# Optimization experiments

Measured on AMD Instinct MI355X. Metric: run time of the kernel, lower is better.

Reference implementation:

```python
import jax, jax.numpy as jnp
import numpy as np

N = 50000      # nodes
E = 800000     # edges (avg degree 16)
D = 128        # d_model
H = 8          # num_heads
DK = D // H    # d_k = 16


def setup_inputs() -> dict:
    key = jax.random.key(0)
    ks = jax.random.split(key, 9)
    scale = np.float32(1.0 / np.sqrt(D))
    return {
        "q": jax.random.normal(ks[0], (N, D), jnp.float32),
        "k": jax.random.normal(ks[1], (N, D), jnp.float32),
        "v": jax.random.normal(ks[2], (N, D), jnp.float32),
        "e": jax.random.normal(ks[3], (E, D), jnp.float32),
        "src": jax.random.randint(ks[4], (E,), 0, N),
        "dst": jax.random.randint(ks[5], (E,), 0, N),
        # nn.Linear(D, D, bias=False) weights, stored as [in, out]
        "Wq": jax.random.normal(ks[6], (D, D), jnp.float32) * scale,
        "Wk": jax.random.normal(ks[7], (D, D), jnp.float32) * scale,
        "Wv": jax.random.normal(ks[8], (D, D), jnp.float32) * scale,
    }


def reference(q, k, v, e, src, dst, Wq, Wk, Wv):
    inv_sqrt_dk = np.float32(1.0 / np.sqrt(DK))
    # node-level V projection, then per-edge gather of src V  -> [E, H, DK]
    Vn = (v @ Wv).reshape(N, H, DK)
    Ve = Vn[src]
    # per-edge Q from dst node, K from (src k + edge feature e)
    Qe = (q[dst] @ Wq).reshape(E, H, DK)
    Ke = ((k[src] + e) @ Wk).reshape(E, H, DK)
    # per-edge HxH score matrix: Q @ K^T / sqrt(d_k), leaky-relu
    s = jnp.einsum("ehd,egd->ehg", Qe, Ke) * inv_sqrt_dk   # [E, H, H]
    s = jax.nn.leaky_relu(s)
    # softmax over last head axis (within each edge, as in reduce_func dim=-1)
    A = jax.nn.softmax(s, axis=-1)
    # per-edge message, heads regrouped -> [E, D]
    He = jnp.einsum("ehg,egd->ehd", A, Ve).reshape(E, D)
    # plain sum over incoming edges per destination node -> [N, D]
    return jax.ops.segment_sum(He, dst, num_segments=N)
```

## Files before the change

kernel.cpp:

```cpp
#include <hip/hip_runtime.h>
#include <hip/hip_bf16.h>
#include <math.h>

#define NN 50000
#define EE 800000
#define DD 128
#define HH 8
#define DKK 16

typedef __attribute__((ext_vector_type(8))) short short8;
typedef __attribute__((ext_vector_type(4))) float f32x4;
typedef __attribute__((ext_vector_type(4))) unsigned short ushort4v;
typedef __attribute__((ext_vector_type(8))) unsigned short ushort8v;

static __device__ __forceinline__ unsigned short f2bf(float x) {
  __hip_bfloat16 h = __float2bfloat16(x);
  return *reinterpret_cast<unsigned short*>(&h);
}
static __device__ __forceinline__ float bf2f(unsigned short u) {
  return __uint_as_float(((unsigned int)u) << 16);
}

__global__ __launch_bounds__(256) void hist_kernel(const int* __restrict__ dst,
                                                   int* __restrict__ cnt) {
  int i4 = blockIdx.x * 256 + threadIdx.x;
  if (i4 < EE / 4) {
    int4 d = *(const int4*)&dst[i4 * 4];
    atomicAdd(&cnt[d.x], 1);
    atomicAdd(&cnt[d.y], 1);
    atomicAdd(&cnt[d.z], 1);
    atomicAdd(&cnt[d.w], 1);
  }
}

#define SCAN_NB ((NN + 1023) / 1024)

__global__ __launch_bounds__(256) void scan1_kernel(const int* __restrict__ cnt,
                                                    int* __restrict__ bsum) {
  __shared__ int red[256];
  const int b = blockIdx.x, t = threadIdx.x;
  const int base = b * 1024 + t * 4;
  int s = 0;
  if (base + 3 < NN) {
    int4 v = *(const int4*)&cnt[base];
    s = v.x + v.y + v.z + v.w;
  } else {
    for (int j = 0; j < 4; ++j) if (base + j < NN) s += cnt[base + j];
  }
  red[t] = s;
  __syncthreads();
  for (int off = 1; off < 256; off <<= 1) {
    int v = (t >= off) ? red[t - off] : 0;
    __syncthreads();
    red[t] += v;
    __syncthreads();
  }
  if (t == 255) bsum[b] = red[255];
}

__global__ __launch_bounds__(256) void scan3_kernel(const int* __restrict__ cnt,
                                                    const int* __restrict__ bsum,
                                                    int* __restrict__ rowptr) {
  __shared__ int red[256];
  __shared__ int bs[SCAN_NB];
  const int b = blockIdx.x, t = threadIdx.x;
  if (t < SCAN_NB) bs[t] = bsum[t];
  const int base = b * 1024 + t * 4;
  int v0 = 0, v1 = 0, v2 = 0, v3 = 0;
  if (base + 3 < NN) {
    int4 v = *(const int4*)&cnt[base];
    v0 = v.x; v1 = v.y; v2 = v.z; v3 = v.w;
  } else {
    if (base + 0 < NN) v0 = cnt[base + 0];
    if (base + 1 < NN) v1 = cnt[base + 1];
    if (base + 2 < NN) v2 = cnt[base + 2];
    if (base + 3 < NN) v3 = cnt[base + 3];
  }
  red[t] = v0 + v1 + v2 + v3;
  __syncthreads();
  for (int off = 1; off < 256; off <<= 1) {
    int v = (t >= off) ? red[t - off] : 0;
    __syncthreads();
    red[t] += v;
    __syncthreads();
  }
  int bpre = 0;
  for (int j = 0; j < b; ++j) bpre += bs[j];
  int r = bpre + ((t == 0) ? 0 : red[t - 1]);
  if (base + 0 < NN) { rowptr[base + 0] = r; r += v0; }
  if (base + 1 < NN) { rowptr[base + 1] = r; r += v1; }
  if (base + 2 < NN) { rowptr[base + 2] = r; r += v2; }
  if (base + 3 < NN) { rowptr[base + 3] = r; }
}

__global__ __launch_bounds__(256) void fill_kernel(const int* __restrict__ dst,
                                                   const int* __restrict__ rowptr,
                                                   int* __restrict__ cur,
                                                   int* __restrict__ perm) {
  int i4 = blockIdx.x * 256 + threadIdx.x;
  if (i4 < EE / 4) {
    int4 dv = *(const int4*)&dst[i4 * 4];
    int d0 = dv.x, d1 = dv.y, d2 = dv.z, d3 = dv.w;
    int s0 = atomicAdd(&cur[d0], 1); perm[rowptr[d0] + s0] = i4 * 4 + 0;
    int s1 = atomicAdd(&cur[d1], 1); perm[rowptr[d1] + s1] = i4 * 4 + 1;
    int s2 = atomicAdd(&cur[d2], 1); perm[rowptr[d2] + s2] = i4 * 4 + 2;
    int s3 = atomicAdd(&cur[d3], 1); perm[rowptr[d3] + s3] = i4 * 4 + 3;
  }
}

__global__ void prep_w_kernel(const float* __restrict__ Wq,
                              const float* __restrict__ Wk,
                              const float* __restrict__ Wv,
                              unsigned short* __restrict__ WqT,
                              unsigned short* __restrict__ WkT,
                              unsigned short* __restrict__ WvT) {
  int c = blockIdx.x & 127;
  int m = blockIdx.x >> 7;
  int j = threadIdx.x;
  const float* W = (m == 0) ? Wq : (m == 1) ? Wk : Wv;
  unsigned short* o = (m == 0) ? WqT : (m == 1) ? WkT : WvT;
  o[j * DD + c] = f2bf(W[c * DD + j]);
}

__global__ __launch_bounds__(512) void node_proj_kernel(
    const float* __restrict__ q, const float* __restrict__ v,
    const float* __restrict__ k,
    const unsigned short* __restrict__ WqT, const unsigned short* __restrict__ WvT,
    unsigned short* __restrict__ Qh, unsigned short* __restrict__ Vh,
    unsigned short* __restrict__ kh)
{
  __shared__ __align__(16) unsigned short xl[64 * 136];
  const int tid = threadIdx.x;
  const int n0 = blockIdx.x * 64;

  #pragma unroll
  for (int p = 0; p < 2; ++p) {
    int f = p * 512 + tid;
    int i = f >> 4, c8 = f & 15;
    int n = n0 + i;
    if (n < NN) {
      float4 a = *(const float4*)&k[(size_t)n * DD + c8 * 8];
      float4 b = *(const float4*)&k[(size_t)n * DD + c8 * 8 + 4];
      ushort8v o = { f2bf(a.x), f2bf(a.y), f2bf(a.z), f2bf(a.w),
                     f2bf(b.x), f2bf(b.y), f2bf(b.z), f2bf(b.w) };
      *(ushort8v*)&kh[(size_t)n * DD + c8 * 8] = o;
    }
  }

  for (int m = 0; m < 2; ++m) {
    const float* x = m ? v : q;
    const unsigned short* WT = m ? WvT : WqT;
    unsigned short* o = m ? Vh : Qh;

    __syncthreads();
    #pragma unroll
    for (int p = 0; p < 4; ++p) {
      int f = p * 512 + tid;
      int i = f >> 5, c4 = f & 31;
      int n = n0 + i;
      float4 t = (n < NN) ? *(const float4*)&x[(size_t)n * DD + c4 * 4]
                          : float4{0.f, 0.f, 0.f, 0.f};
      ushort4v u = { f2bf(t.x), f2bf(t.y), f2bf(t.z), f2bf(t.w) };
      *(ushort4v*)&xl[i * 136 + c4 * 4] = u;
    }
    __syncthreads();

    const int lane = tid & 63, wid = tid >> 6;
    const int rg = wid & 3, cg = wid >> 2;
    const int lr = lane & 15, lg = lane >> 4;

    f32x4 acc0 = {0.f,0.f,0.f,0.f}, acc1 = {0.f,0.f,0.f,0.f};
    f32x4 acc2 = {0.f,0.f,0.f,0.f}, acc3 = {0.f,0.f,0.f,0.f};

    const unsigned short* Ab = &xl[(rg * 16 + lr) * 136];
    const unsigned short* B0 = &WT[(size_t)(cg * 64 +  0 + lr) * DD];
    const unsigned short* B1 = &WT[(size_t)(cg * 64 + 16 + lr) * DD];
    const unsigned short* B2 = &WT[(size_t)(cg * 64 + 32 + lr) * DD];
    const unsigned short* B3 = &WT[(size_t)(cg * 64 + 48 + lr) * DD];

    #pragma unroll
    for (int kk = 0; kk < 4; ++kk) {
      const int kof = kk * 32 + lg * 8;
      short8 a = *(const short8*)(Ab + kof);
      acc0 = __builtin_amdgcn_mfma_f32_16x16x32_bf16(a, *(const short8*)(B0 + kof), acc0, 0, 0, 0);
      acc1 = __builtin_amdgcn_mfma_f32_16x16x32_bf16(a, *(const short8*)(B1 + kof), acc1, 0, 0, 0);
      acc2 = __builtin_amdgcn_mfma_f32_16x16x32_bf16(a, *(const short8*)(B2 + kof), acc2, 0, 0, 0);
      acc3 = __builtin_amdgcn_mfma_f32_16x16x32_bf16(a, *(const short8*)(B3 + kof), acc3, 0, 0, 0);
    }

    const int r0 = rg * 16 + lg * 4;
    const int cb = cg * 64 + lr;
    #pragma unroll
    for (int r = 0; r < 4; ++r) {
      int n = n0 + r0 + r;
      if (n < NN) {
        unsigned short* orow = &o[(size_t)n * DD + cb];
        orow[ 0] = f2bf(acc0[r]);
        orow[16] = f2bf(acc1[r]);
        orow[32] = f2bf(acc2[r]);
        orow[48] = f2bf(acc3[r]);
      }
    }
  }
}

__global__ __launch_bounds__(512, 4) void edge_attn_kernel(
    const unsigned short* __restrict__ kh, const float* __restrict__ e,
    const int* __restrict__ src, const int* __restrict__ dst,
    const int* __restrict__ perm,
    const unsigned short* __restrict__ WkT,
    const unsigned short* __restrict__ Qh, const unsigned short* __restrict__ Vh,
    float* __restrict__ out)
{
  __shared__ __align__(16) unsigned short buf[128 * 136];
  __shared__ __align__(16) unsigned short vbuf[128 * 136];
  __shared__ __align__(16) unsigned short pbuf[8 * 16 * 24];
  __shared__ int s_perm[128], s_src[128], s_dst[128];

  const int tid = threadIdx.x;
  const size_t e0 = (size_t)blockIdx.x * 128;
  const int lane = tid & 63, wid = tid >> 6;
  const int lr = lane & 15, lg = lane >> 4;

  if (tid < 128) {
    int pe = perm[e0 + tid];
    s_perm[tid] = pe;
    s_src[tid] = src[pe];
    s_dst[tid] = dst[pe];
  }
  __syncthreads();

  ushort8v vv[4], kv[4];
  float4 ea[4], eb[4];
  #pragma unroll
  for (int p = 0; p < 4; ++p) {
    int f = p * 512 + tid;
    int i2 = f >> 4, c8 = f & 15;
    vv[p] = *(const ushort8v*)&Vh[(size_t)s_src[i2] * DD + c8 * 8];
    kv[p] = *(const ushort8v*)&kh[(size_t)s_src[i2] * DD + c8 * 8];
    const float* ep = &e[(size_t)s_perm[i2] * DD + c8 * 8];
    ea[p] = *(const float4*)ep;
    eb[p] = *(const float4*)(ep + 4);
  }

  const short8 zero8 = {0, 0, 0, 0, 0, 0, 0, 0};
  const int ebase = wid * 16;
  short8 qf[8];
  #pragma unroll
  for (int j = 0; j < 8; ++j) {
    if (lg < 2) {
      int ie = ebase + 2 * j + (lr >> 3);
      qf[j] = *(const short8*)&Qh[(size_t)s_dst[ie] * DD + (lr & 7) * DKK + lg * 8];
    } else qf[j] = zero8;
  }

  #pragma unroll
  for (int p = 0; p < 4; ++p) {
    int f = p * 512 + tid;
    int i2 = f >> 4, c8 = f & 15;
    *(ushort8v*)&vbuf[i2 * 136 + c8 * 8] = vv[p];
    ushort8v o;
    o[0] = f2bf(bf2f(kv[p][0]) + ea[p].x);
    o[1] = f2bf(bf2f(kv[p][1]) + ea[p].y);
    o[2] = f2bf(bf2f(kv[p][2]) + ea[p].z);
    o[3] = f2bf(bf2f(kv[p][3]) + ea[p].w);
    o[4] = f2bf(bf2f(kv[p][4]) + eb[p].x);
    o[5] = f2bf(bf2f(kv[p][5]) + eb[p].y);
    o[6] = f2bf(bf2f(kv[p][6]) + eb[p].z);
    o[7] = f2bf(bf2f(kv[p][7]) + eb[p].w);
    *(ushort8v*)&buf[i2 * 136 + c8 * 8] = o;
  }
  __syncthreads();

  {
    const int rgA = wid & 3, rgB = (wid & 3) + 4, cg = wid >> 2;

    f32x4 aA0 = {0.f,0.f,0.f,0.f}, aA1 = {0.f,0.f,0.f,0.f};
    f32x4 aA2 = {0.f,0.f,0.f,0.f}, aA3 = {0.f,0.f,0.f,0.f};
    f32x4 aB0 = {0.f,0.f,0.f,0.f}, aB1 = {0.f,0.f,0.f,0.f};
    f32x4 aB2 = {0.f,0.f,0.f,0.f}, aB3 = {0.f,0.f,0.f,0.f};

    const unsigned short* AbA = &buf[(rgA * 16 + lr) * 136];
    const unsigned short* AbB = &buf[(rgB * 16 + lr) * 136];
    const unsigned short* B0 = &WkT[(size_t)(cg * 64 +  0 + lr) * DD];
    const unsigned short* B1 = &WkT[(size_t)(cg * 64 + 16 + lr) * DD];
    const unsigned short* B2 = &WkT[(size_t)(cg * 64 + 32 + lr) * DD];
    const unsigned short* B3 = &WkT[(size_t)(cg * 64 + 48 + lr) * DD];

    #pragma unroll
    for (int kk = 0; kk < 4; ++kk) {
      const int kof = kk * 32 + lg * 8;
      short8 b0 = *(const short8*)(B0 + kof);
      short8 b1 = *(const short8*)(B1 + kof);
      short8 b2 = *(const short8*)(B2 + kof);
      short8 b3 = *(const short8*)(B3 + kof);
      short8 fA = *(const short8*)(AbA + kof);
      short8 fB = *(const short8*)(AbB + kof);
      aA0 = __builtin_amdgcn_mfma_f32_16x16x32_bf16(fA, b0, aA0, 0, 0, 0);
      aA1 = __builtin_amdgcn_mfma_f32_16x16x32_bf16(fA, b1, aA1, 0, 0, 0);
      aA2 = __builtin_amdgcn_mfma_f32_16x16x32_bf16(fA, b2, aA2, 0, 0, 0);
      aA3 = __builtin_amdgcn_mfma_f32_16x16x32_bf16(fA, b3, aA3, 0, 0, 0);
      aB0 = __builtin_amdgcn_mfma_f32_16x16x32_bf16(fB, b0, aB0, 0, 0, 0);
      aB1 = __builtin_amdgcn_mfma_f32_16x16x32_bf16(fB, b1, aB1, 0, 0, 0);
      aB2 = __builtin_amdgcn_mfma_f32_16x16x32_bf16(fB, b2, aB2, 0, 0, 0);
      aB3 = __builtin_amdgcn_mfma_f32_16x16x32_bf16(fB, b3, aB3, 0, 0, 0);
    }

    __syncthreads();

    const int rA = rgA * 16 + lg * 4;
    const int rB = rgB * 16 + lg * 4;
    const int cb = cg * 64 + lr;
    #pragma unroll
    for (int r = 0; r < 4; ++r) {
      buf[(rA + r) * 136 + cb +  0] = f2bf(aA0[r]);
      buf[(rA + r) * 136 + cb + 16] = f2bf(aA1[r]);
      buf[(rA + r) * 136 + cb + 32] = f2bf(aA2[r]);
      buf[(rA + r) * 136 + cb + 48] = f2bf(aA3[r]);
      buf[(rB + r) * 136 + cb +  0] = f2bf(aB0[r]);
      buf[(rB + r) * 136 + cb + 16] = f2bf(aB1[r]);
      buf[(rB + r) * 136 + cb + 32] = f2bf(aB2[r]);
      buf[(rB + r) * 136 + cb + 48] = f2bf(aB3[r]);
    }
  }
  __syncthreads();

  {
    const bool valid = ((lr < 8) == (lg < 2));
    unsigned short* pb = &pbuf[wid * 16 * 24];

    #pragma unroll
    for (int j = 0; j < 8; ++j) {
      const int iea = ebase + 2 * j, ieb = iea + 1;

      short8 af = zero8;
      if (lg < 2) {
        int ie = (lr < 8) ? iea : ieb;
        af = *(const short8*)&buf[ie * 136 + (lr & 7) * DKK + lg * 8];
      }
      f32x4 c = {0.f, 0.f, 0.f, 0.f};
      c = __builtin_amdgcn_mfma_f32_16x16x32_bf16(af, qf[j], c, 0, 0, 0);

      float s0, s1, s2, s3;
      {
        float x0 = c[0] * 0.25f, x1 = c[1] * 0.25f;
        float x2 = c[2] * 0.25f, x3 = c[3] * 0.25f;
        x0 = (x0 >= 0.f) ? x0 : 0.01f * x0;
        x1 = (x1 >= 0.f) ? x1 : 0.01f * x1;
        x2 = (x2 >= 0.f) ? x2 : 0.01f * x2;
        x3 = (x3 >= 0.f) ? x3 : 0.01f * x3;
        s0 = valid ? x0 : -1e30f;
        s1 = valid ? x1 : -1e30f;
        s2 = valid ? x2 : -1e30f;
        s3 = valid ? x3 : -1e30f;
      }
      float m = fmaxf(fmaxf(s0, s1), fmaxf(s2, s3));
      m = fmaxf(m, __shfl_xor(m, 16));
      m = fmaxf(m, __shfl_xor(m, 32));
      float p0 = __expf(s0 - m), p1 = __expf(s1 - m);
      float p2 = __expf(s2 - m), p3 = __expf(s3 - m);
      float su = p0 + p1 + p2 + p3;
      su += __shfl_xor(su, 16);
      su += __shfl_xor(su, 32);
      float rs = 1.0f / su;

      ushort4v pk = { f2bf(p0 * rs), f2bf(p1 * rs), f2bf(p2 * rs), f2bf(p3 * rs) };
      *(ushort4v*)&pb[lr * 24 + lg * 4] = pk;

      short8 pa = zero8;
      if (lg < 2) pa = *(const short8*)&pb[lr * 24 + lg * 8];
      short8 vf = zero8;
      if (lg < 2) {
        const unsigned short* vr = &vbuf[(lg ? ieb : iea) * 136 + lr];
        vf[0] = (short)vr[0 * 16];
        vf[1] = (short)vr[1 * 16];
        vf[2] = (short)vr[2 * 16];
        vf[3] = (short)vr[3 * 16];
        vf[4] = (short)vr[4 * 16];
        vf[5] = (short)vr[5 * 16];
        vf[6] = (short)vr[6 * 16];
        vf[7] = (short)vr[7 * 16];
      }
      f32x4 hc = {0.f, 0.f, 0.f, 0.f};
      hc = __builtin_amdgcn_mfma_f32_16x16x32_bf16(pa, vf, hc, 0, 0, 0);

      #pragma unroll
      for (int r = 0; r < 4; ++r) {
        int rr = lg * 4 + r;
        int ie = (rr < 8) ? iea : ieb;
        buf[ie * 136 + (rr & 7) * DKK + lr] = f2bf(hc[r]);
      }
    }
  }

  {
    const int d2 = lane;
    const int base = ebase;
    float s0 = 0.0f, s1 = 0.0f;
    int curd = s_dst[base];
    #pragma unroll 8
    for (int j = 0; j < 16; ++j) {
      int i2 = base + j;
      int dn2 = s_dst[i2];
      if (dn2 != curd) {
        atomicAdd(&out[(size_t)curd * DD + d2 * 2],     s0);
        atomicAdd(&out[(size_t)curd * DD + d2 * 2 + 1], s1);
        s0 = 0.0f; s1 = 0.0f;
        curd = dn2;
      }
      unsigned int w = *(const unsigned int*)&buf[i2 * 136 + d2 * 2];
      s0 += bf2f((unsigned short)(w & 0xffff));
      s1 += bf2f((unsigned short)(w >> 16));
    }
    atomicAdd(&out[(size_t)curd * DD + d2 * 2],     s0);
    atomicAdd(&out[(size_t)curd * DD + d2 * 2 + 1], s1);
  }
}

extern "C" void kernel_launch(void* const* d_in, const int* in_sizes, int n_in,
                              void* d_out, int out_size, void* d_ws, size_t ws_size,
                              hipStream_t stream) {
  const float* q  = (const float*)d_in[0];
  const float* k  = (const float*)d_in[1];
  const float* v  = (const float*)d_in[2];
  const float* e  = (const float*)d_in[3];
  const int*   src = (const int*)d_in[4];
  const int*   dst = (const int*)d_in[5];
  const float* Wq = (const float*)d_in[6];
  const float* Wk = (const float*)d_in[7];
  const float* Wv = (const float*)d_in[8];

  float* out = (float*)d_out;
  char* wsb = (char*)d_ws;
  unsigned short* Qh  = (unsigned short*)wsb;
  unsigned short* Vh  = Qh + (size_t)NN * DD;
  unsigned short* kh  = Vh + (size_t)NN * DD;
  unsigned short* WqT = kh + (size_t)NN * DD;
  unsigned short* WkT = WqT + DD * DD;
  unsigned short* WvT = WkT + DD * DD;
  int* cnt    = (int*)(WvT + DD * DD);
  int* cur    = cnt + NN;
  int* rowptr = cur + NN;
  int* bsum   = rowptr + NN + 1;
  int* perm   = bsum + 64;

  hipMemsetAsync(d_out, 0, (size_t)NN * DD * sizeof(float), stream);
  hipMemsetAsync(cnt, 0, 2 * NN * sizeof(int), stream);

  hist_kernel <<<(EE / 4 + 255) / 256, 256, 0, stream>>>(dst, cnt);
  scan1_kernel<<<SCAN_NB, 256, 0, stream>>>(cnt, bsum);
  scan3_kernel<<<SCAN_NB, 256, 0, stream>>>(cnt, bsum, rowptr);
  fill_kernel <<<(EE / 4 + 255) / 256, 256, 0, stream>>>(dst, rowptr, cur, perm);

  prep_w_kernel<<<3 * DD, DD, 0, stream>>>(Wq, Wk, Wv, WqT, WkT, WvT);
  node_proj_kernel<<<(NN + 63) / 64, 512, 0, stream>>>(q, v, k, WqT, WvT,
                                                       Qh, Vh, kh);
  edge_attn_kernel<<<EE / 128, 512, 0, stream>>>(kh, e, src, dst, perm,
                                                 WkT, Qh, Vh, out);
}
```

Measured before the change: 384.5 us.

## Halve edge tile to 64 per block and fuse gather with K+e store

The edge attention kernel now processes 64 edges per 512-thread block instead of 128. Shared memory per block halves and the launch-bounds occupancy hint is dropped. The gather loop writes V and K+e into shared memory right away instead of holding all loads in registers first, which lowers register pressure. In exchange each block reuses the WkT tile over fewer edges, segment runs for the atomic reductions are shorter, and there are twice as many blocks.

After: 416.2 us. +8.2%, slower.

```diff
diff --git a/kernel.cpp b/kernel.cpp
--- a/kernel.cpp
+++ b/kernel.cpp
@@ -204,7 +204,7 @@
   }
 }
 
-__global__ __launch_bounds__(512, 4) void edge_attn_kernel(
+__global__ __launch_bounds__(512) void edge_attn_kernel(
     const unsigned short* __restrict__ kh, const float* __restrict__ e,
     const int* __restrict__ src, const int* __restrict__ dst,
     const int* __restrict__ perm,
@@ -212,17 +212,17 @@
     const unsigned short* __restrict__ Qh, const unsigned short* __restrict__ Vh,
     float* __restrict__ out)
 {
-  __shared__ __align__(16) unsigned short buf[128 * 136];
-  __shared__ __align__(16) unsigned short vbuf[128 * 136];
+  __shared__ __align__(16) unsigned short buf[64 * 136];
+  __shared__ __align__(16) unsigned short vbuf[64 * 136];
   __shared__ __align__(16) unsigned short pbuf[8 * 16 * 24];
-  __shared__ int s_perm[128], s_src[128], s_dst[128];
+  __shared__ int s_perm[64], s_src[64], s_dst[64];
 
   const int tid = threadIdx.x;
-  const size_t e0 = (size_t)blockIdx.x * 128;
+  const size_t e0 = (size_t)blockIdx.x * 64;
   const int lane = tid & 63, wid = tid >> 6;
   const int lr = lane & 15, lg = lane >> 4;
 
-  if (tid < 128) {
+  if (tid < 64) {
     int pe = perm[e0 + tid];
     s_perm[tid] = pe;
     s_src[tid] = src[pe];
@@ -230,58 +230,47 @@
   }
   __syncthreads();
 
-  ushort8v vv[4], kv[4];
-  float4 ea[4], eb[4];
   #pragma unroll
-  for (int p = 0; p < 4; ++p) {
+  for (int p = 0; p < 2; ++p) {
     int f = p * 512 + tid;
     int i2 = f >> 4, c8 = f & 15;
-    vv[p] = *(const ushort8v*)&Vh[(size_t)s_src[i2] * DD + c8 * 8];
-    kv[p] = *(const ushort8v*)&kh[(size_t)s_src[i2] * DD + c8 * 8];
+    ushort8v vv = *(const ushort8v*)&Vh[(size_t)s_src[i2] * DD + c8 * 8];
+    ushort8v kv = *(const ushort8v*)&kh[(size_t)s_src[i2] * DD + c8 * 8];
     const float* ep = &e[(size_t)s_perm[i2] * DD + c8 * 8];
-    ea[p] = *(const float4*)ep;
-    eb[p] = *(const float4*)(ep + 4);
+    float4 ea = *(const float4*)ep;
+    float4 eb = *(const float4*)(ep + 4);
+    *(ushort8v*)&vbuf[i2 * 136 + c8 * 8] = vv;
+    ushort8v o;
+    o[0] = f2bf(bf2f(kv[0]) + ea.x);
+    o[1] = f2bf(bf2f(kv[1]) + ea.y);
+    o[2] = f2bf(bf2f(kv[2]) + ea.z);
+    o[3] = f2bf(bf2f(kv[3]) + ea.w);
+    o[4] = f2bf(bf2f(kv[4]) + eb.x);
+    o[5] = f2bf(bf2f(kv[5]) + eb.y);
+    o[6] = f2bf(bf2f(kv[6]) + eb.z);
+    o[7] = f2bf(bf2f(kv[7]) + eb.w);
+    *(ushort8v*)&buf[i2 * 136 + c8 * 8] = o;
   }
 
   const short8 zero8 = {0, 0, 0, 0, 0, 0, 0, 0};
-  const int ebase = wid * 16;
-  short8 qf[8];
+  const int ebase = wid * 8;
+  short8 qf[4];
   #pragma unroll
-  for (int j = 0; j < 8; ++j) {
+  for (int j = 0; j < 4; ++j) {
     if (lg < 2) {
       int ie = ebase + 2 * j + (lr >> 3);
       qf[j] = *(const short8*)&Qh[(size_t)s_dst[ie] * DD + (lr & 7) * DKK + lg * 8];
     } else qf[j] = zero8;
   }
-
-  #pragma unroll
-  for (int p = 0; p < 4; ++p) {
-    int f = p * 512 + tid;
-    int i2 = f >> 4, c8 = f & 15;
-    *(ushort8v*)&vbuf[i2 * 136 + c8 * 8] = vv[p];
-    ushort8v o;
-    o[0] = f2bf(bf2f(kv[p][0]) + ea[p].x);
-    o[1] = f2bf(bf2f(kv[p][1]) + ea[p].y);
-    o[2] = f2bf(bf2f(kv[p][2]) + ea[p].z);
-    o[3] = f2bf(bf2f(kv[p][3]) + ea[p].w);
-    o[4] = f2bf(bf2f(kv[p][4]) + eb[p].x);
-    o[5] = f2bf(bf2f(kv[p][5]) + eb[p].y);
-    o[6] = f2bf(bf2f(kv[p][6]) + eb[p].z);
-    o[7] = f2bf(bf2f(kv[p][7]) + eb[p].w);
-    *(ushort8v*)&buf[i2 * 136 + c8 * 8] = o;
-  }
   __syncthreads();
 
   {
-    const int rgA = wid & 3, rgB = (wid & 3) + 4, cg = wid >> 2;
-
-    f32x4 aA0 = {0.f,0.f,0.f,0.f}, aA1 = {0.f,0.f,0.f,0.f};
-    f32x4 aA2 = {0.f,0.f,0.f,0.f}, aA3 = {0.f,0.f,0.f,0.f};
-    f32x4 aB0 = {0.f,0.f,0.f,0.f}, aB1 = {0.f,0.f,0.f,0.f};
-    f32x4 aB2 = {0.f,0.f,0.f,0.f}, aB3 = {0.f,0.f,0.f,0.f};
-
-    const unsigned short* AbA = &buf[(rgA * 16 + lr) * 136];
-    const unsigned short* AbB = &buf[(rgB * 16 + lr) * 136];
+    const int rg = wid & 3, cg = wid >> 2;
+
+    f32x4 a0 = {0.f,0.f,0.f,0.f}, a1 = {0.f,0.f,0.f,0.f};
+    f32x4 a2 = {0.f,0.f,0.f,0.f}, a3 = {0.f,0.f,0.f,0.f};
+
+    const unsigned short* Ab = &buf[(rg * 16 + lr) * 136];
     const unsigned short* B0 = &WkT[(size_t)(cg * 64 +  0 + lr) * DD];
     const unsigned short* B1 = &WkT[(size_t)(cg * 64 + 16 + lr) * DD];
     const unsigned short* B2 = &WkT[(size_t)(cg * 64 + 32 + lr) * DD];
@@ -290,37 +279,23 @@
     #pragma unroll
     for (int kk = 0; kk < 4; ++kk) {
       const int kof = kk * 32 + lg * 8;
-      short8 b0 = *(const short8*)(B0 + kof);
-      short8 b1 = *(const short8*)(B1 + kof);
-      short8 b2 = *(const short8*)(B2 + kof);
-      short8 b3 = *(const short8*)(B3 + kof);
-      short8 fA = *(const short8*)(AbA + kof);
-      short8 fB = *(const short8*)(AbB + kof);
-      aA0 = __builtin_amdgcn_mfma_f32_16x16x32_bf16(fA, b0, aA0, 0, 0, 0);
-      aA1 = __builtin_amdgcn_mfma_f32_16x16x32_bf16(fA, b1, aA1, 0, 0, 0);
-      aA2 = __builtin_amdgcn_mfma_f32_16x16x32_bf16(fA, b2, aA2, 0, 0, 0);
-      aA3 = __builtin_amdgcn_mfma_f32_16x16x32_bf16(fA, b3, aA3, 0, 0, 0);
-      aB0 = __builtin_amdgcn_mfma_f32_16x16x32_bf16(fB, b0, aB0, 0, 0, 0);
-      aB1 = __builtin_amdgcn_mfma_f32_16x16x32_bf16(fB, b1, aB1, 0, 0, 0);
-      aB2 = __builtin_amdgcn_mfma_f32_16x16x32_bf16(fB, b2, aB2, 0, 0, 0);
-      aB3 = __builtin_amdgcn_mfma_f32_16x16x32_bf16(fB, b3, aB3, 0, 0, 0);
-    }
-
-    __syncthreads();
-
-    const int rA = rgA * 16 + lg * 4;
-    const int rB = rgB * 16 + lg * 4;
+      short8 a = *(const short8*)(Ab + kof);
+      a0 = __builtin_amdgcn_mfma_f32_16x16x32_bf16(a, *(const short8*)(B0 + kof), a0, 0, 0, 0);
+      a1 = __builtin_amdgcn_mfma_f32_16x16x32_bf16(a, *(const short8*)(B1 + kof), a1, 0, 0, 0);
+      a2 = __builtin_amdgcn_mfma_f32_16x16x32_bf16(a, *(const short8*)(B2 + kof), a2, 0, 0, 0);
+      a3 = __builtin_amdgcn_mfma_f32_16x16x32_bf16(a, *(const short8*)(B3 + kof), a3, 0, 0, 0);
+    }
+
+    __syncthreads();
+
+    const int r0 = rg * 16 + lg * 4;
     const int cb = cg * 64 + lr;
     #pragma unroll
     for (int r = 0; r < 4; ++r) {
-      buf[(rA + r) * 136 + cb +  0] = f2bf(aA0[r]);
-      buf[(rA + r) * 136 + cb + 16] = f2bf(aA1[r]);
-      buf[(rA + r) * 136 + cb + 32] = f2bf(aA2[r]);
-      buf[(rA + r) * 136 + cb + 48] = f2bf(aA3[r]);
-      buf[(rB + r) * 136 + cb +  0] = f2bf(aB0[r]);
-      buf[(rB + r) * 136 + cb + 16] = f2bf(aB1[r]);
-      buf[(rB + r) * 136 + cb + 32] = f2bf(aB2[r]);
-      buf[(rB + r) * 136 + cb + 48] = f2bf(aB3[r]);
+      buf[(r0 + r) * 136 + cb +  0] = f2bf(a0[r]);
+      buf[(r0 + r) * 136 + cb + 16] = f2bf(a1[r]);
+      buf[(r0 + r) * 136 + cb + 32] = f2bf(a2[r]);
+      buf[(r0 + r) * 136 + cb + 48] = f2bf(a3[r]);
     }
   }
   __syncthreads();
@@ -330,7 +305,7 @@
     unsigned short* pb = &pbuf[wid * 16 * 24];
 
     #pragma unroll
-    for (int j = 0; j < 8; ++j) {
+    for (int j = 0; j < 4; ++j) {
       const int iea = ebase + 2 * j, ieb = iea + 1;
 
       short8 af = zero8;
@@ -395,12 +370,11 @@
 
   {
     const int d2 = lane;
-    const int base = ebase;
     float s0 = 0.0f, s1 = 0.0f;
-    int curd = s_dst[base];
+    int curd = s_dst[ebase];
     #pragma unroll 8
-    for (int j = 0; j < 16; ++j) {
-      int i2 = base + j;
+    for (int j = 0; j < 8; ++j) {
+      int i2 = ebase + j;
       int dn2 = s_dst[i2];
       if (dn2 != curd) {
         atomicAdd(&out[(size_t)curd * DD + d2 * 2],     s0);
@@ -455,6 +429,6 @@
   prep_w_kernel<<<3 * DD, DD, 0, stream>>>(Wq, Wk, Wv, WqT, WkT, WvT);
   node_proj_kernel<<<(NN + 63) / 64, 512, 0, stream>>>(q, v, k, WqT, WvT,
                                                        Qh, Vh, kh);
-  edge_attn_kernel<<<EE / 128, 512, 0, stream>>>(kh, e, src, dst, perm,
-                                                 WkT, Qh, Vh, out);
-}
+  edge_attn_kernel<<<EE / 64, 512, 0, stream>>>(kh, e, src, dst, perm,
+                                                WkT, Qh, Vh, out);
+}
```

## Process edges in original order and scatter messages for CSR segmented reduce

Applied to the files above, without the earlier changes.

When the workspace is large enough, the edge kernel reads edges in their original order, so the e rows stream sequentially instead of being gathered through perm. Each edge's bf16 message is written to its dst-sorted slot in a staging buffer, and a new reduce kernel sums each node's rows through rowptr with no atomics and no output memset. The cost is an extra write and read of a 200 MB bf16 buffer in exchange for contiguous e reads and no float atomics. It also drops the occupancy hint on launch bounds and folds the staging loop into the gather loop.

Result: slower. 498.4 us (+29.6%).

```diff
diff --git a/kernel.cpp b/kernel.cpp
--- a/kernel.cpp
+++ b/kernel.cpp
@@ -91,20 +91,30 @@
   if (base + 1 < NN) { rowptr[base + 1] = r; r += v1; }
   if (base + 2 < NN) { rowptr[base + 2] = r; r += v2; }
   if (base + 3 < NN) { rowptr[base + 3] = r; }
+  if (b == SCAN_NB - 1 && t == 255) {
+    int tot = 0;
+    for (int j = 0; j < SCAN_NB; ++j) tot += bs[j];
+    rowptr[NN] = tot;
+  }
 }
 
 __global__ __launch_bounds__(256) void fill_kernel(const int* __restrict__ dst,
                                                    const int* __restrict__ rowptr,
                                                    int* __restrict__ cur,
-                                                   int* __restrict__ perm) {
+                                                   int* __restrict__ perm,
+                                                   int* __restrict__ pos) {
   int i4 = blockIdx.x * 256 + threadIdx.x;
   if (i4 < EE / 4) {
     int4 dv = *(const int4*)&dst[i4 * 4];
     int d0 = dv.x, d1 = dv.y, d2 = dv.z, d3 = dv.w;
-    int s0 = atomicAdd(&cur[d0], 1); perm[rowptr[d0] + s0] = i4 * 4 + 0;
-    int s1 = atomicAdd(&cur[d1], 1); perm[rowptr[d1] + s1] = i4 * 4 + 1;
-    int s2 = atomicAdd(&cur[d2], 1); perm[rowptr[d2] + s2] = i4 * 4 + 2;
-    int s3 = atomicAdd(&cur[d3], 1); perm[rowptr[d3] + s3] = i4 * 4 + 3;
+    int s0 = atomicAdd(&cur[d0], 1); int p0 = rowptr[d0] + s0;
+    int s1 = atomicAdd(&cur[d1], 1); int p1 = rowptr[d1] + s1;
+    int s2 = atomicAdd(&cur[d2], 1); int p2 = rowptr[d2] + s2;
+    int s3 = atomicAdd(&cur[d3], 1); int p3 = rowptr[d3] + s3;
+    perm[p0] = i4 * 4 + 0; perm[p1] = i4 * 4 + 1;
+    perm[p2] = i4 * 4 + 2; perm[p3] = i4 * 4 + 3;
+    int4 pv = { p0, p1, p2, p3 };
+    *(int4*)&pos[i4 * 4] = pv;
   }
 }
 
@@ -204,18 +214,19 @@
   }
 }
 
-__global__ __launch_bounds__(512, 4) void edge_attn_kernel(
+template<int SCATTER>
+__global__ __launch_bounds__(512) void edge_attn_kernel(
     const unsigned short* __restrict__ kh, const float* __restrict__ e,
     const int* __restrict__ src, const int* __restrict__ dst,
-    const int* __restrict__ perm,
+    const int* __restrict__ perm, const int* __restrict__ pos,
     const unsigned short* __restrict__ WkT,
     const unsigned short* __restrict__ Qh, const unsigned short* __restrict__ Vh,
-    float* __restrict__ out)
+    float* __restrict__ out, unsigned short* __restrict__ Hes)
 {
   __shared__ __align__(16) unsigned short buf[128 * 136];
   __shared__ __align__(16) unsigned short vbuf[128 * 136];
   __shared__ __align__(16) unsigned short pbuf[8 * 16 * 24];
-  __shared__ int s_perm[128], s_src[128], s_dst[128];
+  __shared__ int s_perm[128], s_src[128], s_dst[128], s_pos[128];
 
   const int tid = threadIdx.x;
   const size_t e0 = (size_t)blockIdx.x * 128;
@@ -223,24 +234,34 @@
   const int lr = lane & 15, lg = lane >> 4;
 
   if (tid < 128) {
-    int pe = perm[e0 + tid];
-    s_perm[tid] = pe;
-    s_src[tid] = src[pe];
-    s_dst[tid] = dst[pe];
+    int ge = SCATTER ? (int)(e0 + tid) : perm[e0 + tid];
+    s_perm[tid] = ge;
+    s_src[tid] = src[ge];
+    s_dst[tid] = dst[ge];
+    if (SCATTER) s_pos[tid] = pos[e0 + tid];
   }
   __syncthreads();
 
-  ushort8v vv[4], kv[4];
-  float4 ea[4], eb[4];
   #pragma unroll
   for (int p = 0; p < 4; ++p) {
     int f = p * 512 + tid;
     int i2 = f >> 4, c8 = f & 15;
-    vv[p] = *(const ushort8v*)&Vh[(size_t)s_src[i2] * DD + c8 * 8];
-    kv[p] = *(const ushort8v*)&kh[(size_t)s_src[i2] * DD + c8 * 8];
+    ushort8v vv = *(const ushort8v*)&Vh[(size_t)s_src[i2] * DD + c8 * 8];
+    ushort8v kv = *(const ushort8v*)&kh[(size_t)s_src[i2] * DD + c8 * 8];
     const float* ep = &e[(size_t)s_perm[i2] * DD + c8 * 8];
-    ea[p] = *(const float4*)ep;
-    eb[p] = *(const float4*)(ep + 4);
+    float4 ea = *(const float4*)ep;
+    float4 eb = *(const float4*)(ep + 4);
+    *(ushort8v*)&vbuf[i2 * 136 + c8 * 8] = vv;
+    ushort8v o;
+    o[0] = f2bf(bf2f(kv[0]) + ea.x);
+    o[1] = f2bf(bf2f(kv[1]) + ea.y);
+    o[2] = f2bf(bf2f(kv[2]) + ea.z);
+    o[3] = f2bf(bf2f(kv[3]) + ea.w);
+    o[4] = f2bf(bf2f(kv[4]) + eb.x);
+    o[5] = f2bf(bf2f(kv[5]) + eb.y);
+    o[6] = f2bf(bf2f(kv[6]) + eb.z);
+    o[7] = f2bf(bf2f(kv[7]) + eb.w);
+    *(ushort8v*)&buf[i2 * 136 + c8 * 8] = o;
   }
 
   const short8 zero8 = {0, 0, 0, 0, 0, 0, 0, 0};
@@ -252,23 +273,6 @@
       int ie = ebase + 2 * j + (lr >> 3);
       qf[j] = *(const short8*)&Qh[(size_t)s_dst[ie] * DD + (lr & 7) * DKK + lg * 8];
     } else qf[j] = zero8;
-  }
-
-  #pragma unroll
-  for (int p = 0; p < 4; ++p) {
-    int f = p * 512 + tid;
-    int i2 = f >> 4, c8 = f & 15;
-    *(ushort8v*)&vbuf[i2 * 136 + c8 * 8] = vv[p];
-    ushort8v o;
-    o[0] = f2bf(bf2f(kv[p][0]) + ea[p].x);
-    o[1] = f2bf(bf2f(kv[p][1]) + ea[p].y);
-    o[2] = f2bf(bf2f(kv[p][2]) + ea[p].z);
-    o[3] = f2bf(bf2f(kv[p][3]) + ea[p].w);
-    o[4] = f2bf(bf2f(kv[p][4]) + eb[p].x);
-    o[5] = f2bf(bf2f(kv[p][5]) + eb[p].y);
-    o[6] = f2bf(bf2f(kv[p][6]) + eb[p].z);
-    o[7] = f2bf(bf2f(kv[p][7]) + eb[p].w);
-    *(ushort8v*)&buf[i2 * 136 + c8 * 8] = o;
   }
   __syncthreads();
 
@@ -393,14 +397,21 @@
     }
   }
 
-  {
+  if (SCATTER) {
+    #pragma unroll
+    for (int jj = 0; jj < 4; ++jj) {
+      int i2 = ebase + jj * 4 + (lane >> 4);
+      int c8 = lane & 15;
+      *(ushort8v*)&Hes[(size_t)s_pos[i2] * DD + c8 * 8] =
+          *(const ushort8v*)&buf[i2 * 136 + c8 * 8];
+    }
+  } else {
     const int d2 = lane;
-    const int base = ebase;
     float s0 = 0.0f, s1 = 0.0f;
-    int curd = s_dst[base];
+    int curd = s_dst[ebase];
     #pragma unroll 8
     for (int j = 0; j < 16; ++j) {
-      int i2 = base + j;
+      int i2 = ebase + j;
       int dn2 = s_dst[i2];
       if (dn2 != curd) {
         atomicAdd(&out[(size_t)curd * DD + d2 * 2],     s0);
@@ -415,6 +426,25 @@
     atomicAdd(&out[(size_t)curd * DD + d2 * 2],     s0);
     atomicAdd(&out[(size_t)curd * DD + d2 * 2 + 1], s1);
   }
+}
+
+__global__ __launch_bounds__(256) void reduce_kernel(
+    const unsigned short* __restrict__ Hes, const int* __restrict__ rowptr,
+    float* __restrict__ out)
+{
+  int n = blockIdx.x * 2 + (threadIdx.x >> 7);
+  int d = threadIdx.x & 127;
+  if (n >= NN) return;
+  int r0 = rowptr[n], r1 = rowptr[n + 1];
+  float s = 0.f;
+  int j = r0;
+  for (; j + 1 < r1; j += 2) {
+    float a = bf2f(Hes[(size_t)j * DD + d]);
+    float b = bf2f(Hes[(size_t)(j + 1) * DD + d]);
+    s += a + b;
+  }
+  if (j < r1) s += bf2f(Hes[(size_t)j * DD + d]);
+  out[(size_t)n * DD + d] = s;
 }
 
 extern "C" void kernel_launch(void* const* d_in, const int* in_sizes, int n_in,
@@ -443,18 +473,30 @@
   int* rowptr = cur + NN;
   int* bsum   = rowptr + NN + 1;
   int* perm   = bsum + 64;
-
-  hipMemsetAsync(d_out, 0, (size_t)NN * DD * sizeof(float), stream);
+  int* pos    = perm + EE;
+  size_t hoff = ((size_t)((char*)(pos + EE) - wsb) + 15) & ~(size_t)15;
+  unsigned short* Hes = (unsigned short*)(wsb + hoff);
+  size_t need = hoff + (size_t)EE * DD * sizeof(unsigned short);
+  const bool scatter = (ws_size >= need);
+
   hipMemsetAsync(cnt, 0, 2 * NN * sizeof(int), stream);
 
   hist_kernel <<<(EE / 4 + 255) / 256, 256, 0, stream>>>(dst, cnt);
   scan1_kernel<<<SCAN_NB, 256, 0, stream>>>(cnt, bsum);
   scan3_kernel<<<SCAN_NB, 256, 0, stream>>>(cnt, bsum, rowptr);
-  fill_kernel <<<(EE / 4 + 255) / 256, 256, 0, stream>>>(dst, rowptr, cur, perm);
+  fill_kernel <<<(EE / 4 + 255) / 256, 256, 0, stream>>>(dst, rowptr, cur,
+                                                         perm, pos);
 
   prep_w_kernel<<<3 * DD, DD, 0, stream>>>(Wq, Wk, Wv, WqT, WkT, WvT);
   node_proj_kernel<<<(NN + 63) / 64, 512, 0, stream>>>(q, v, k, WqT, WvT,
                                                        Qh, Vh, kh);
-  edge_attn_kernel<<<EE / 128, 512, 0, stream>>>(kh, e, src, dst, perm,
-                                                 WkT, Qh, Vh, out);
-}
+  if (scatter) {
+    edge_attn_kernel<1><<<EE / 128, 512, 0, stream>>>(
+        kh, e, src, dst, perm, pos, WkT, Qh, Vh, out, Hes);
+    reduce_kernel<<<(NN + 1) / 2, 256, 0, stream>>>(Hes, rowptr, out);
+  } else {
+    hipMemsetAsync(d_out, 0, (size_t)NN * DD * sizeof(float), stream);
+    edge_attn_kernel<0><<<EE / 128, 512, 0, stream>>>(
+        kh, e, src, dst, perm, pos, WkT, Qh, Vh, out, Hes);
+  }
+}
```
